# Kernel tuning notes

Measured on AMD Instinct MI355X. Metric: run time of the kernel, lower is better.

Reference implementation:

```python
import jax, jax.numpy as jnp
import numpy as np

N = 12288
NUM_GRAPHS = 64


def setup_inputs() -> dict:
    key = jax.random.key(0)
    k1, k2, k3 = jax.random.split(key, 3)
    scores = jax.random.normal(k1, (N,), dtype=jnp.float32)
    labels = jax.random.randint(k2, (N,), 0, 2, dtype=jnp.int32)
    segment_ids = jnp.sort(jax.random.randint(k3, (N,), 0, NUM_GRAPHS, dtype=jnp.int32))
    return {"scores": scores, "labels": labels, "segment_ids": segment_ids}


def reference(scores, labels, segment_ids):
    # Pair (i, j) is valid iff: same graph, label[i] == 1 (pos), label[j] == 0 (neg).
    lab = labels.astype(jnp.bool_)
    same_graph = segment_ids[:, None] == segment_ids[None, :]          # [N, N]
    mask = same_graph & lab[:, None] & (~lab)[None, :]                 # [N, N]
    diff = scores[:, None] - scores[None, :]                           # s_pos - s_neg
    hinge = jnp.maximum(1.0 - diff, 0.0)
    total = jnp.sum(jnp.where(mask, hinge, 0.0))
    cnt = jnp.sum(mask).astype(scores.dtype)
    # mean over all pairs; zero loss (== mean(scores*0)) if no pairs exist
    loss = jnp.where(cnt > 0, total / jnp.maximum(cnt, 1.0), jnp.zeros((), scores.dtype))
    return loss
```

## Files before the change

### kernel.cpp

```cpp
#include <hip/hip_runtime.h>


#define NUM_GRAPHS 64
#define BLOCK 256
#define CAP 6144

__device__ __forceinline__ int lower_bound_i(const int* __restrict__ a, int n, int v) {
    int lo = 0, hi = n;
    while (lo < hi) {
        int mid = (lo + hi) >> 1;
        if (a[mid] < v) lo = mid + 1; else hi = mid;
    }
    return lo;
}

__global__ __launch_bounds__(BLOCK)
void pairwise_per_graph(const float* __restrict__ scores,
                        const int* __restrict__ labels,
                        const int* __restrict__ seg,
                        int n,
                        float* __restrict__ tots,
                        long long* __restrict__ cnts) {
    __shared__ float s_pos[CAP];
    __shared__ float s_neg[CAP];
    __shared__ float sm[BLOCK / 64];
    __shared__ int cp, cn;
    __shared__ unsigned long long sh_cnt;

    const int g   = blockIdx.x;
    const int tid = threadIdx.x;

    const int start = lower_bound_i(seg, n, g);
    const int end   = lower_bound_i(seg, n, g + 1);

    if (tid == 0) { cp = 0; cn = 0; sh_cnt = 0ull; }
    __syncthreads();

    for (int i = start + tid; i < end; i += BLOCK) {
        float s = scores[i];
        if (labels[i] != 0) {
            int p = atomicAdd(&cp, 1);
            if (p < CAP) s_pos[p] = s;
        } else {
            int p = atomicAdd(&cn, 1);
            if (p < CAP) s_neg[p] = s;
        }
    }
    __syncthreads();

    const int np = cp;
    const int nn = cn;

    float local = 0.0f;
    unsigned long long pairs = 0ull;

    if (np <= CAP && nn <= CAP) {
        for (int p = tid; p < np; p += BLOCK) {
            const float base = 1.0f - s_pos[p];
            for (int j = 0; j < nn; ++j) {
                local += fmaxf(base + s_neg[j], 0.0f);
            }
        }
        if (tid == 0) pairs = (unsigned long long)np * (unsigned long long)nn;
    } else {
        for (int i = start + tid; i < end; i += BLOCK) {
            if (labels[i] != 0) {
                const float base = 1.0f - scores[i];
                for (int j = start; j < end; ++j) {
                    if (labels[j] == 0) {
                        local += fmaxf(base + scores[j], 0.0f);
                        pairs++;
                    }
                }
            }
        }
    }

    if (pairs) atomicAdd(&sh_cnt, pairs);

    for (int off = 32; off; off >>= 1) local += __shfl_down(local, off, 64);
    const int wave = tid >> 6, lane = tid & 63;
    if (lane == 0) sm[wave] = local;
    __syncthreads();

    if (tid == 0) {
        float tot = 0.0f;
        #pragma unroll
        for (int w = 0; w < BLOCK / 64; ++w) tot += sm[w];
        tots[g] = tot;
        cnts[g] = (long long)sh_cnt;
    }
}

__global__ __launch_bounds__(64)
void pairwise_finalize(const long long* __restrict__ cnts,
                       const float* __restrict__ tots,
                       float* __restrict__ out) {
    const int t = threadIdx.x;
    float tot = tots[t];
    long long c = cnts[t];
    for (int off = 32; off; off >>= 1) {
        tot += __shfl_down(tot, off, 64);
        c   += __shfl_down(c,   off, 64);
    }
    if (t == 0) {
        out[0] = (c > 0) ? (tot / (float)c) : 0.0f;
    }
}

extern "C" void kernel_launch(void* const* d_in, const int* in_sizes, int n_in,
                              void* d_out, int out_size, void* d_ws, size_t ws_size,
                              hipStream_t stream) {
    const float* scores = (const float*)d_in[0];
    const int*   labels = (const int*)d_in[1];
    const int*   seg    = (const int*)d_in[2];
    float*       out    = (float*)d_out;
    const int n = in_sizes[0];

    long long* cnts = (long long*)d_ws;
    float*     tots = (float*)((char*)d_ws + NUM_GRAPHS * sizeof(long long));

    pairwise_per_graph<<<NUM_GRAPHS, BLOCK, 0, stream>>>(scores, labels, seg, n, tots, cnts);
    pairwise_finalize<<<1, 64, 0, stream>>>(cnts, tots, out);
}
```

Measured before the change: 64.95 us.

## Fuse finalize into per-graph kernel with ballot-based segment search and compaction

Replaces the serial binary search for segment bounds with a sampled ballot search, switches shared-memory compaction from per-thread atomics to wave-aggregated ballot/popcount offsets, unrolls the inner hinge loop by four, and folds the finalize kernel into the main kernel using global atomics and a last-block ticket. A memset of the workspace is added before the launch. Float atomic accumulation across blocks makes the summation order nondeterministic, and CAP is reduced to 4096, which pushes larger graphs onto the slow fallback path.

New measurement: 66.76 us. +2.8%, slower.

```diff
diff --git a/kernel.cpp b/kernel.cpp
--- a/kernel.cpp
+++ b/kernel.cpp
@@ -3,63 +3,104 @@
 
 #define NUM_GRAPHS 64
 #define BLOCK 256
-#define CAP 6144
-
-__device__ __forceinline__ int lower_bound_i(const int* __restrict__ a, int n, int v) {
-    int lo = 0, hi = n;
-    while (lo < hi) {
-        int mid = (lo + hi) >> 1;
-        if (a[mid] < v) lo = mid + 1; else hi = mid;
-    }
-    return lo;
-}
+#define CAP 4096
 
 __global__ __launch_bounds__(BLOCK)
-void pairwise_per_graph(const float* __restrict__ scores,
-                        const int* __restrict__ labels,
-                        const int* __restrict__ seg,
-                        int n,
-                        float* __restrict__ tots,
-                        long long* __restrict__ cnts) {
+void pairwise_fused(const float* __restrict__ scores,
+                    const int* __restrict__ labels,
+                    const int* __restrict__ seg,
+                    int n,
+                    float* __restrict__ g_tot,
+                    unsigned long long* __restrict__ g_cnt,
+                    unsigned int* __restrict__ g_done,
+                    float* __restrict__ out) {
     __shared__ float s_pos[CAP];
     __shared__ float s_neg[CAP];
+    __shared__ int s_cp, s_cn, s_loA, s_loB, s_start, s_end;
     __shared__ float sm[BLOCK / 64];
-    __shared__ int cp, cn;
-    __shared__ unsigned long long sh_cnt;
+    __shared__ unsigned long long smc[BLOCK / 64];
 
-    const int g   = blockIdx.x;
-    const int tid = threadIdx.x;
+    const int g    = blockIdx.x;
+    const int tid  = threadIdx.x;
+    const int lane = tid & 63;
+    const int wave = tid >> 6;
+    const unsigned long long below = (1ull << lane) - 1ull;
 
-    const int start = lower_bound_i(seg, n, g);
-    const int end   = lower_bound_i(seg, n, g + 1);
-
-    if (tid == 0) { cp = 0; cn = 0; sh_cnt = 0ull; }
+    if (tid == 0) { s_cp = 0; s_cn = 0; s_loA = -1; s_loB = -1; s_start = 0; s_end = 0; }
     __syncthreads();
 
-    for (int i = start + tid; i < end; i += BLOCK) {
-        float s = scores[i];
-        if (labels[i] != 0) {
-            int p = atomicAdd(&cp, 1);
-            if (p < CAP) s_pos[p] = s;
-        } else {
-            int p = atomicAdd(&cn, 1);
-            if (p < CAP) s_neg[p] = s;
+    const int stride = (n + BLOCK - 1) / BLOCK;
+    if (stride <= 64) {
+        int pos = tid * stride;
+        int v = (pos < n) ? seg[pos] : 0x7fffffff;
+        unsigned long long mA = __ballot(v < g);
+        unsigned long long mB = __ballot(v < g + 1);
+        if (mA && lane == 63 - __clzll(mA)) atomicMax(&s_loA, pos);
+        if (mB && lane == 63 - __clzll(mB)) atomicMax(&s_loB, pos);
+        __syncthreads();
+
+        if (wave == 0) {
+            int L = s_loA;
+            int idx = L + 1 + lane;
+            bool pred = (lane < stride) && (idx < n) && (seg[idx] < g);
+            unsigned long long m = __ballot(pred);
+            if (lane == 0) s_start = L + 1 + __popcll(m);
+        } else if (wave == 1) {
+            int L = s_loB;
+            int idx = L + 1 + lane;
+            bool pred = (lane < stride) && (idx < n) && (seg[idx] < g + 1);
+            unsigned long long m = __ballot(pred);
+            if (lane == 0) s_end = L + 1 + __popcll(m);
+        }
+    } else {
+        if (tid == 0) {
+            int lo = 0, hi = n;
+            while (lo < hi) { int m = (lo + hi) >> 1; if (seg[m] < g) lo = m + 1; else hi = m; }
+            s_start = lo;
+            lo = 0; hi = n;
+            while (lo < hi) { int m = (lo + hi) >> 1; if (seg[m] < g + 1) lo = m + 1; else hi = m; }
+            s_end = lo;
         }
     }
     __syncthreads();
+    const int start = s_start, end = s_end;
 
-    const int np = cp;
-    const int nn = cn;
+    for (int bi = start + wave * 64; bi < end; bi += BLOCK) {
+        int i = bi + lane;
+        bool valid = i < end;
+        int   lab = valid ? labels[i] : 0;
+        float sc  = valid ? scores[i] : 0.0f;
+        bool isp = valid && (lab != 0);
+        bool isn = valid && (lab == 0);
+        unsigned long long pm = __ballot(isp);
+        unsigned long long nm = __ballot(isn);
+        int pb = 0, nb = 0;
+        if (lane == 0) {
+            pb = atomicAdd(&s_cp, __popcll(pm));
+            nb = atomicAdd(&s_cn, __popcll(nm));
+        }
+        pb = __shfl(pb, 0, 64);
+        nb = __shfl(nb, 0, 64);
+        if (isp) { int r = pb + __popcll(pm & below); if (r < CAP) s_pos[r] = sc; }
+        else if (isn) { int r = nb + __popcll(nm & below); if (r < CAP) s_neg[r] = sc; }
+    }
+    __syncthreads();
 
+    const int np = s_cp, nn = s_cn;
     float local = 0.0f;
     unsigned long long pairs = 0ull;
 
     if (np <= CAP && nn <= CAP) {
         for (int p = tid; p < np; p += BLOCK) {
             const float base = 1.0f - s_pos[p];
-            for (int j = 0; j < nn; ++j) {
-                local += fmaxf(base + s_neg[j], 0.0f);
+            int j = 0;
+            for (; j + 4 <= nn; j += 4) {
+                local += fmaxf(base + s_neg[j],     0.0f);
+                local += fmaxf(base + s_neg[j + 1], 0.0f);
+                local += fmaxf(base + s_neg[j + 2], 0.0f);
+                local += fmaxf(base + s_neg[j + 3], 0.0f);
             }
+            for (; j < nn; ++j) local += fmaxf(base + s_neg[j], 0.0f);
         }
         if (tid == 0) pairs = (unsigned long long)np * (unsigned long long)nn;
     } else {
@@ -67,44 +108,33 @@
             if (labels[i] != 0) {
                 const float base = 1.0f - scores[i];
                 for (int j = start; j < end; ++j) {
-                    if (labels[j] == 0) {
-                        local += fmaxf(base + scores[j], 0.0f);
-                        pairs++;
-                    }
+                    if (labels[j] == 0) { local += fmaxf(base + scores[j], 0.0f); pairs++; }
                 }
             }
         }
     }
 
-    if (pairs) atomicAdd(&sh_cnt, pairs);
-
-    for (int off = 32; off; off >>= 1) local += __shfl_down(local, off, 64);
-    const int wave = tid >> 6, lane = tid & 63;
-    if (lane == 0) sm[wave] = local;
+    for (int off = 32; off; off >>= 1) {
+        local += __shfl_down(local, off, 64);
+        pairs += __shfl_down(pairs, off, 64);
+    }
+    if (lane == 0) { sm[wave] = local; smc[wave] = pairs; }
     __syncthreads();
 
     if (tid == 0) {
         float tot = 0.0f;
+        unsigned long long c = 0ull;
         #pragma unroll
-        for (int w = 0; w < BLOCK / 64; ++w) tot += sm[w];
-        tots[g] = tot;
-        cnts[g] = (long long)sh_cnt;
-    }
-}
-
-__global__ __launch_bounds__(64)
-void pairwise_finalize(const long long* __restrict__ cnts,
-                       const float* __restrict__ tots,
-                       float* __restrict__ out) {
-    const int t = threadIdx.x;
-    float tot = tots[t];
-    long long c = cnts[t];
-    for (int off = 32; off; off >>= 1) {
-        tot += __shfl_down(tot, off, 64);
-        c   += __shfl_down(c,   off, 64);
-    }
-    if (t == 0) {
-        out[0] = (c > 0) ? (tot / (float)c) : 0.0f;
+        for (int w = 0; w < BLOCK / 64; ++w) { tot += sm[w]; c += smc[w]; }
+        atomicAdd(g_tot, tot);
+        atomicAdd(g_cnt, c);
+        __threadfence();
+        unsigned int ticket = atomicAdd(g_done, 1u);
+        if (ticket == gridDim.x - 1) {
+            float T = atomicAdd(g_tot, 0.0f);
+            unsigned long long C = atomicAdd(g_cnt, 0ull);
+            out[0] = (C > 0) ? (T / (float)C) : 0.0f;
+        }
     }
 }
 
@@ -117,9 +147,11 @@
     float*       out    = (float*)d_out;
     const int n = in_sizes[0];
 
-    long long* cnts = (long long*)d_ws;
-    float*     tots = (float*)((char*)d_ws + NUM_GRAPHS * sizeof(long long));
+    float*              g_tot  = (float*)d_ws;
+    unsigned long long* g_cnt  = (unsigned long long*)((char*)d_ws + 8);
+    unsigned int*       g_done = (unsigned int*)((char*)d_ws + 16);
 
-    pairwise_per_graph<<<NUM_GRAPHS, BLOCK, 0, stream>>>(scores, labels, seg, n, tots, cnts);
-    pairwise_finalize<<<1, 64, 0, stream>>>(cnts, tots, out);
+    hipMemsetAsync(d_ws, 0, 24, stream);
+    pairwise_fused<<<NUM_GRAPHS, BLOCK, 0, stream>>>(scores, labels, seg, n,
+                                                     g_tot, g_cnt, g_done, out);
 }
```
